# Kernel tuning notes

Measured on AMD Instinct MI355X. Metric: run time of the kernel, lower is better.

## Reference

```python
import jax, jax.numpy as jnp
import numpy as np

D_MODEL = 1024
NUM_HEADS = 16
D_HEAD = D_MODEL // NUM_HEADS
BATCH = 2
SEQ = 2048


def setup_inputs() -> dict:
    key = jax.random.key(0)
    ks = jax.random.split(key, 5)
    std = 0.02
    return {
        "x": jax.random.normal(ks[0], (BATCH, SEQ, D_MODEL), dtype=jnp.float32),
        "Wq": jax.random.normal(ks[1], (D_MODEL, D_MODEL), dtype=jnp.float32) * std,
        "Wk": jax.random.normal(ks[2], (D_MODEL, D_MODEL), dtype=jnp.float32) * std,
        "Wv": jax.random.normal(ks[3], (D_MODEL, D_MODEL), dtype=jnp.float32) * std,
        "Wo": jax.random.normal(ks[4], (D_MODEL, D_MODEL), dtype=jnp.float32) * std,
    }


def reference(x, Wq, Wk, Wv, Wo):
    batch, seq_len, d_model = x.shape
    h, dh = NUM_HEADS, D_HEAD

    def split_heads(W):
        # x @ W.T -> (b, s, d) -> (b, h, s, dh)
        p = jnp.einsum('bsd,ed->bse', x, W)
        return p.reshape(batch, seq_len, h, dh).transpose(0, 2, 1, 3)

    Q = split_heads(Wq)
    K = split_heads(Wk)
    V = split_heads(Wv)

    scale = 1.0 / jnp.sqrt(jnp.asarray(dh, dtype=x.dtype))
    scores = jnp.einsum('bhqd,bhkd->bhqk', Q, K) * scale
    causal = jnp.tril(jnp.ones((seq_len, seq_len), dtype=bool))
    scores = jnp.where(causal, scores, -jnp.inf)
    attn = jax.nn.softmax(scores, axis=-1)
    out = jnp.einsum('bhqk,bhkd->bhqd', attn, V)  # (b, h, s, dh)
    out = out.transpose(0, 2, 1, 3).reshape(batch, seq_len, d_model)
    return jnp.einsum('bsd,ed->bse', out, Wo)
```

## Files before the change

kernel.cpp:

```cpp
#include <hip/hip_runtime.h>

#define D_MODEL 1024
#define NUM_HEADS 16
#define D_HEAD 64
#define BATCH 2
#define SEQ 2048
#define MTOT (BATCH * SEQ)
#define PLANE ((size_t)MTOT * D_MODEL)
#define QSCALE 0.1803368801f

typedef unsigned short us;
typedef __bf16 bf16x8 __attribute__((ext_vector_type(8)));
typedef float floatx4 __attribute__((ext_vector_type(4)));

__device__ __forceinline__ unsigned int f2bf(float f) {
  union { float f; unsigned int i; } v; v.f = f;
  unsigned int r = v.i + 0x7FFFu + ((v.i >> 16) & 1u);
  return r >> 16;
}
__device__ __forceinline__ unsigned int f2bf_tr(float f) {
  union { float f; unsigned int i; } v; v.f = f;
  return v.i >> 16;
}

__global__ __launch_bounds__(256) void convert_all(const float* __restrict__ x,
                                                   const float* __restrict__ Wq,
                                                   const float* __restrict__ Wk,
                                                   const float* __restrict__ Wv,
                                                   const float* __restrict__ Wo,
                                                   us* __restrict__ xbf,
                                                   us* __restrict__ Wqkv,
                                                   us* __restrict__ Wobf) {
  const int i = blockIdx.x * 256 + threadIdx.x;
  const float* src;
  us* dst;
  if (i < (1 << 20)) {
    src = x + (size_t)i * 4;
    dst = xbf + (size_t)i * 4;
  } else {
    const int j = i - (1 << 20);
    const int w = j >> 18;
    const int o = j & ((1 << 18) - 1);
    if (w < 3) {
      const float* ws = (w == 0) ? Wq : (w == 1) ? Wk : Wv;
      src = ws + (size_t)o * 4;
      dst = Wqkv + (size_t)w * (D_MODEL * D_MODEL) + (size_t)o * 4;
    } else {
      src = Wo + (size_t)o * 4;
      dst = Wobf + (size_t)o * 4;
    }
  }
  float4 v = *(const float4*)src;
  uint2 pk;
  pk.x = f2bf(v.x) | (f2bf(v.y) << 16);
  pk.y = f2bf(v.z) | (f2bf(v.w) << 16);
  *(uint2*)dst = pk;
}

template <int CMODE>
__global__ __launch_bounds__(256) void gemm_mfma(const us* __restrict__ A,
                                                 const us* __restrict__ B,
                                                 void* __restrict__ Cv,
                                                 int M, int N, int K) {
  __shared__ __bf16 As[2][128 * 32];
  __shared__ __bf16 Bs[2][128 * 32];
  const int tid = threadIdx.x;
  const int wid = tid >> 6;
  const int lane = tid & 63;
  const int bm = blockIdx.y * 128;
  const int bn = blockIdx.x * 128;
  const int wm = (wid & 1) * 64;
  const int wn = (wid >> 1) * 64;
  const int lr = lane & 15;
  const int quad = lane >> 4;

  floatx4 acc[4][4] = {};
  const int cb0 = wid * 128;

  auto stage = [&](int buf, int k0) {
#pragma unroll
    for (int p = 0; p < 2; ++p) {
      const int cb = cb0 + p * 64;
      const int c = cb + lane;
      const us* ga = A + (size_t)(bm + (c >> 2)) * K + (k0 + (c & 3) * 8);
      const us* gb = B + (size_t)(bn + (c >> 2)) * K + (k0 + (c & 3) * 8);
      __builtin_amdgcn_global_load_lds((const __attribute__((address_space(1))) void*)ga,
                                       (__attribute__((address_space(3))) void*)(&As[buf][cb * 8]),
                                       16, 0, 0);
      __builtin_amdgcn_global_load_lds((const __attribute__((address_space(1))) void*)gb,
                                       (__attribute__((address_space(3))) void*)(&Bs[buf][cb * 8]),
                                       16, 0, 0);
    }
  };

  stage(0, 0);
  __syncthreads();

  int cur = 0;
  for (int k0 = 0; k0 < K; k0 += 32) {
    if (k0 + 32 < K) stage(cur ^ 1, k0 + 32);

    bf16x8 a[4], b[4];
#pragma unroll
    for (int i = 0; i < 4; ++i)
      a[i] = *(const bf16x8*)&As[cur][(wm + i * 16 + lr) * 32 + quad * 8];
#pragma unroll
    for (int j = 0; j < 4; ++j)
      b[j] = *(const bf16x8*)&Bs[cur][(wn + j * 16 + lr) * 32 + quad * 8];
#pragma unroll
    for (int i = 0; i < 4; ++i)
#pragma unroll
      for (int j = 0; j < 4; ++j)
        acc[i][j] = __builtin_amdgcn_mfma_f32_16x16x32_bf16(a[i], b[j], acc[i][j], 0, 0, 0);

    __syncthreads();
    cur ^= 1;
  }

#pragma unroll
  for (int i = 0; i < 4; ++i) {
#pragma unroll
    for (int j = 0; j < 4; ++j) {
      const int col = bn + wn + j * 16 + lr;
      if constexpr (CMODE == 1) {
        us* dst = (us*)Cv;
        const int plane = col >> 10;
        if (plane < 2) {
          const float s = (plane == 0) ? QSCALE : 1.0f;
#pragma unroll
          for (int r = 0; r < 4; ++r) {
            const int row = bm + wm + i * 16 + quad * 4 + r;
            dst[(size_t)plane * PLANE + (size_t)row * 1024 + (col & 1023)] =
                (us)f2bf(acc[i][j][r] * s);
          }
        } else {
          const int d = col & 63;
          const int hh = (col >> 6) & 15;
          const int row0 = bm + wm + i * 16 + quad * 4;
          const int bb = row0 >> 11;
          const int ss = row0 & 2047;
          uint2 pk;
          pk.x = f2bf(acc[i][j][0]) | (f2bf(acc[i][j][1]) << 16);
          pk.y = f2bf(acc[i][j][2]) | (f2bf(acc[i][j][3]) << 16);
          *(uint2*)&dst[2 * PLANE + ((size_t)((bb * 16 + hh) * 64 + d)) * 2048 + ss] = pk;
        }
      } else {
#pragma unroll
        for (int r = 0; r < 4; ++r) {
          const int row = bm + wm + i * 16 + quad * 4 + r;
          ((float*)Cv)[(size_t)row * N + col] = acc[i][j][r];
        }
      }
    }
  }
}

#define ASTR 72

__global__ __launch_bounds__(512, 2) void attn_mfma(const us* __restrict__ Qb,
                                                    const us* __restrict__ Kb,
                                                    const us* __restrict__ Vtg,
                                                    us* __restrict__ Ob) {
  const int bx = blockIdx.x;
  const int b = bx >> 8;
  const int idx = bx & 255;
  const int h = idx >> 4;
  const int s0 = idx & 15;
  const int strip = b ? (15 - s0) : s0;
  const int q0 = strip * 128;
  const int ntiles = 2 * strip + 2;
  const int tid = threadIdx.x;
  const int w = tid >> 6;
  const int lane = tid & 63;
  const int lr = lane & 15;
  const int quad = lane >> 4;

  __shared__ us Ks[2][64 * ASTR];
  __shared__ us Vs[2][64 * ASTR];
  __shared__ us Ps[8 * 16 * ASTR];

  const us* kbase = Kb + (size_t)(b * SEQ) * D_MODEL + h * D_HEAD;
  const us* vbase = Vtg + (size_t)((b * 16 + h) * 64) * 2048;
  us* const pg = &Ps[w * 16 * ASTR];

  const int grow = q0 + w * 16;
  const us* qp = Qb + (size_t)(b * SEQ + grow + lr) * D_MODEL + h * D_HEAD;
  const bf16x8 qa0 = *(const bf16x8*)(qp + quad * 8);
  const bf16x8 qa1 = *(const bf16x8*)(qp + 32 + quad * 8);

  floatx4 oacc[4] = {};
  floatx4 lacc = {};
  bf16x8 ones;
#pragma unroll
  for (int i = 0; i < 8; ++i) ones[i] = (__bf16)1.0f;

  const int srow = tid >> 3;
  const int schunk = tid & 7;

  uint4 kreg, vreg;
  kreg = *(const uint4*)(kbase + (size_t)srow * D_MODEL + schunk * 8);
  vreg = *(const uint4*)(vbase + (size_t)srow * 2048 + schunk * 8);
  *(uint4*)&Ks[0][srow * ASTR + schunk * 8] = kreg;
  *(uint4*)&Vs[0][srow * ASTR + schunk * 8] = vreg;
  __syncthreads();

  for (int t = 0; t < ntiles; ++t) {
    const int k0 = t * 64;
    const int cur = t & 1;
    const bool more = (t + 1 < ntiles);

    if (more) {
      const int kn = k0 + 64;
      kreg = *(const uint4*)(kbase + (size_t)(kn + srow) * D_MODEL + schunk * 8);
      vreg = *(const uint4*)(vbase + (size_t)srow * 2048 + kn + schunk * 8);
    }

#pragma unroll
    for (int jt = 0; jt < 4; ++jt) {
      const bf16x8 kb0 = *(const bf16x8*)&Ks[cur][(jt * 16 + lr) * ASTR + quad * 8];
      const bf16x8 kb1 = *(const bf16x8*)&Ks[cur][(jt * 16 + lr) * ASTR + 32 + quad * 8];
      floatx4 s = {};
      s = __builtin_amdgcn_mfma_f32_16x16x32_bf16(kb0, qa0, s, 0, 0, 0);
      s = __builtin_amdgcn_mfma_f32_16x16x32_bf16(kb1, qa1, s, 0, 0, 0);
      const int kb = k0 + jt * 16 + quad * 4;
      const bool needMask = (k0 + jt * 16 + 15 > grow);
      float p[4];
#pragma unroll
      for (int r = 0; r < 4; ++r) {
        float e = __builtin_amdgcn_exp2f(s[r]);
        if (needMask && (kb + r > grow + lr)) e = 0.f;
        p[r] = e;
      }
      uint2 pk;
      pk.x = f2bf_tr(p[0]) | (f2bf_tr(p[1]) << 16);
      pk.y = f2bf_tr(p[2]) | (f2bf_tr(p[3]) << 16);
      *(uint2*)&pg[lr * ASTR + jt * 16 + quad * 4] = pk;
    }

    const bf16x8 pa0 = *(const bf16x8*)&pg[lr * ASTR + quad * 8];
    const bf16x8 pa1 = *(const bf16x8*)&pg[lr * ASTR + 32 + quad * 8];
    lacc = __builtin_amdgcn_mfma_f32_16x16x32_bf16(ones, pa0, lacc, 0, 0, 0);
    lacc = __builtin_amdgcn_mfma_f32_16x16x32_bf16(ones, pa1, lacc, 0, 0, 0);
#pragma unroll
    for (int nt = 0; nt < 4; ++nt) {
      const bf16x8 vb0 = *(const bf16x8*)&Vs[cur][(nt * 16 + lr) * ASTR + quad * 8];
      const bf16x8 vb1 = *(const bf16x8*)&Vs[cur][(nt * 16 + lr) * ASTR + 32 + quad * 8];
      oacc[nt] = __builtin_amdgcn_mfma_f32_16x16x32_bf16(vb0, pa0, oacc[nt], 0, 0, 0);
      oacc[nt] = __builtin_amdgcn_mfma_f32_16x16x32_bf16(vb1, pa1, oacc[nt], 0, 0, 0);
    }

    if (more) {
      const int nxt = cur ^ 1;
      *(uint4*)&Ks[nxt][srow * ASTR + schunk * 8] = kreg;
      *(uint4*)&Vs[nxt][srow * ASTR + schunk * 8] = vreg;
    }
    __syncthreads();
  }

  const float inv = 1.f / lacc[0];
#pragma unroll
  for (int nt = 0; nt < 4; ++nt) {
    uint2 pk;
    pk.x = f2bf_tr(oacc[nt][0] * inv) | (f2bf_tr(oacc[nt][1] * inv) << 16);
    pk.y = f2bf_tr(oacc[nt][2] * inv) | (f2bf_tr(oacc[nt][3] * inv) << 16);
    *(uint2*)&pg[lr * ASTR + nt * 16 + quad * 4] = pk;
  }
#pragma unroll
  for (int p = 0; p < 2; ++p) {
    const int c = lane + 64 * p;
    *(uint4*)(Ob + (size_t)(b * SEQ + grow + (c >> 3)) * D_MODEL + h * D_HEAD + (c & 7) * 8) =
        *(const uint4*)&pg[(c >> 3) * ASTR + (c & 7) * 8];
  }
}

extern "C" void kernel_launch(void* const* d_in, const int* in_sizes, int n_in,
                              void* d_out, int out_size, void* d_ws, size_t ws_size,
                              hipStream_t stream) {
  const float* x  = (const float*)d_in[0];
  const float* Wq = (const float*)d_in[1];
  const float* Wk = (const float*)d_in[2];
  const float* Wv = (const float*)d_in[3];
  const float* Wo = (const float*)d_in[4];

  us* xbf = (us*)d_ws;
  us* Qb  = xbf + PLANE;
  us* Kb  = xbf + 2 * PLANE;
  us* Vt  = xbf + 3 * PLANE;
  us* Wobf = xbf + 4 * PLANE;
  us* Ab  = xbf;
  us* Wqkv = (us*)d_out;
  float* out = (float*)d_out;

  convert_all<<<8192, 256, 0, stream>>>(x, Wq, Wk, Wv, Wo, xbf, Wqkv, Wobf);

  gemm_mfma<1><<<dim3(3072 / 128, MTOT / 128), 256, 0, stream>>>(xbf, Wqkv, Qb, MTOT, 3072, D_MODEL);

  attn_mfma<<<512, 512, 0, stream>>>(Qb, Kb, Vt, Ab);

  gemm_mfma<2><<<dim3(D_MODEL / 128, MTOT / 128), 256, 0, stream>>>(Ab, Wobf, out, MTOT, D_MODEL, D_MODEL);
}
```

Measured before the change: 175.7 us.

## Split attention KV range across block pairs with atomic-flag combine

Each attention block now handles a 256-row query strip (two 16-row groups per wave) over half of its causal KV tiles. Two blocks share a strip, write fp32 partial outputs and row sums to workspace, and the second to finish (found through an atomic counter) adds the partner's partials and normalizes. This is meant to balance work across blocks and reuse each K/V tile load for twice as many query rows. The cost is extra global traffic for the partials, flag resets in the convert kernel, and more registers per thread under a raised occupancy hint.

```diff
diff --git a/kernel.cpp b/kernel.cpp
--- a/kernel.cpp
+++ b/kernel.cpp
@@ -30,8 +30,10 @@
                                                    const float* __restrict__ Wo,
                                                    us* __restrict__ xbf,
                                                    us* __restrict__ Wqkv,
-                                                   us* __restrict__ Wobf) {
+                                                   us* __restrict__ Wobf,
+                                                   int* __restrict__ flags) {
   const int i = blockIdx.x * 256 + threadIdx.x;
+  if (blockIdx.x == 0) flags[threadIdx.x] = 0;
   const float* src;
   us* dst;
   if (i < (1 << 20)) {
@@ -157,18 +159,25 @@
 
 #define ASTR 72
 
-__global__ __launch_bounds__(512, 2) void attn_mfma(const us* __restrict__ Qb,
+__global__ __launch_bounds__(512, 4) void attn_mfma(const us* __restrict__ Qb,
                                                     const us* __restrict__ Kb,
                                                     const us* __restrict__ Vtg,
-                                                    us* __restrict__ Ob) {
+                                                    us* __restrict__ Ob,
+                                                    float* __restrict__ Opart,
+                                                    float* __restrict__ Lpart,
+                                                    int* __restrict__ Flags) {
   const int bx = blockIdx.x;
   const int b = bx >> 8;
   const int idx = bx & 255;
   const int h = idx >> 4;
-  const int s0 = idx & 15;
-  const int strip = b ? (15 - s0) : s0;
-  const int q0 = strip * 128;
-  const int ntiles = 2 * strip + 2;
+  const int jj = idx & 15;
+  const int s0 = jj >> 1;
+  const int half = jj & 1;
+  const int strip = b ? (7 - s0) : s0;
+  const int q0 = strip * 256;
+  const int T = 4 * (strip + 1);
+  const int t0 = half * (T >> 1);
+  const int t1 = t0 + (T >> 1);
   const int tid = threadIdx.x;
   const int w = tid >> 6;
   const int lane = tid & 63;
@@ -177,19 +186,30 @@
 
   __shared__ us Ks[2][64 * ASTR];
   __shared__ us Vs[2][64 * ASTR];
-  __shared__ us Ps[8 * 16 * ASTR];
+  __shared__ us Ps[8 * 2 * 16 * ASTR];
+  __shared__ int amCombiner;
 
   const us* kbase = Kb + (size_t)(b * SEQ) * D_MODEL + h * D_HEAD;
   const us* vbase = Vtg + (size_t)((b * 16 + h) * 64) * 2048;
-  us* const pg = &Ps[w * 16 * ASTR];
-
-  const int grow = q0 + w * 16;
-  const us* qp = Qb + (size_t)(b * SEQ + grow + lr) * D_MODEL + h * D_HEAD;
-  const bf16x8 qa0 = *(const bf16x8*)(qp + quad * 8);
-  const bf16x8 qa1 = *(const bf16x8*)(qp + 32 + quad * 8);
-
-  floatx4 oacc[4] = {};
-  floatx4 lacc = {};
+  us* const pg0 = &Ps[(w * 2 + 0) * 16 * ASTR];
+  us* const pg1 = &Ps[(w * 2 + 1) * 16 * ASTR];
+
+  const size_t pairIdx = (size_t)((b * 16 + h) * 8 + strip);
+  float* const Op = Opart + (pairIdx * 2 + half) * (64 * 256);
+  float* const Lp = Lpart + (pairIdx * 2 + half) * 256;
+  const float* const pOp = Opart + (pairIdx * 2 + (half ^ 1)) * (64 * 256);
+  const float* const pLp = Lpart + (pairIdx * 2 + (half ^ 1)) * 256;
+
+  bf16x8 qa[2][2];
+#pragma unroll
+  for (int g = 0; g < 2; ++g) {
+    const us* qp = Qb + (size_t)(b * SEQ + q0 + w * 32 + g * 16 + lr) * D_MODEL + h * D_HEAD;
+    qa[g][0] = *(const bf16x8*)(qp + quad * 8);
+    qa[g][1] = *(const bf16x8*)(qp + 32 + quad * 8);
+  }
+
+  floatx4 oacc[2][4] = {};
+  floatx4 lacc[2] = {};
   bf16x8 ones;
 #pragma unroll
   for (int i = 0; i < 8; ++i) ones[i] = (__bf16)1.0f;
@@ -198,16 +218,16 @@
   const int schunk = tid & 7;
 
   uint4 kreg, vreg;
-  kreg = *(const uint4*)(kbase + (size_t)srow * D_MODEL + schunk * 8);
-  vreg = *(const uint4*)(vbase + (size_t)srow * 2048 + schunk * 8);
+  kreg = *(const uint4*)(kbase + (size_t)(t0 * 64 + srow) * D_MODEL + schunk * 8);
+  vreg = *(const uint4*)(vbase + (size_t)srow * 2048 + t0 * 64 + schunk * 8);
   *(uint4*)&Ks[0][srow * ASTR + schunk * 8] = kreg;
   *(uint4*)&Vs[0][srow * ASTR + schunk * 8] = vreg;
   __syncthreads();
 
-  for (int t = 0; t < ntiles; ++t) {
+  for (int t = t0; t < t1; ++t) {
     const int k0 = t * 64;
-    const int cur = t & 1;
-    const bool more = (t + 1 < ntiles);
+    const int cur = (t - t0) & 1;
+    const bool more = (t + 1 < t1);
 
     if (more) {
       const int kn = k0 + 64;
@@ -219,34 +239,45 @@
     for (int jt = 0; jt < 4; ++jt) {
       const bf16x8 kb0 = *(const bf16x8*)&Ks[cur][(jt * 16 + lr) * ASTR + quad * 8];
       const bf16x8 kb1 = *(const bf16x8*)&Ks[cur][(jt * 16 + lr) * ASTR + 32 + quad * 8];
-      floatx4 s = {};
-      s = __builtin_amdgcn_mfma_f32_16x16x32_bf16(kb0, qa0, s, 0, 0, 0);
-      s = __builtin_amdgcn_mfma_f32_16x16x32_bf16(kb1, qa1, s, 0, 0, 0);
-      const int kb = k0 + jt * 16 + quad * 4;
-      const bool needMask = (k0 + jt * 16 + 15 > grow);
-      float p[4];
-#pragma unroll
-      for (int r = 0; r < 4; ++r) {
-        float e = __builtin_amdgcn_exp2f(s[r]);
-        if (needMask && (kb + r > grow + lr)) e = 0.f;
-        p[r] = e;
+#pragma unroll
+      for (int g = 0; g < 2; ++g) {
+        floatx4 s = {};
+        s = __builtin_amdgcn_mfma_f32_16x16x32_bf16(kb0, qa[g][0], s, 0, 0, 0);
+        s = __builtin_amdgcn_mfma_f32_16x16x32_bf16(kb1, qa[g][1], s, 0, 0, 0);
+        const int grow = q0 + w * 32 + g * 16;
+        const int kb = k0 + jt * 16 + quad * 4;
+        const bool needMask = (k0 + jt * 16 + 15 > grow);
+        float p[4];
+#pragma unroll
+        for (int r = 0; r < 4; ++r) {
+          float e = __builtin_amdgcn_exp2f(s[r]);
+          if (needMask && (kb + r > grow + lr)) e = 0.f;
+          p[r] = e;
+        }
+        uint2 pk;
+        pk.x = f2bf_tr(p[0]) | (f2bf_tr(p[1]) << 16);
+        pk.y = f2bf_tr(p[2]) | (f2bf_tr(p[3]) << 16);
+        us* const pg = g ? pg1 : pg0;
+        *(uint2*)&pg[lr * ASTR + jt * 16 + quad * 4] = pk;
       }
-      uint2 pk;
-      pk.x = f2bf_tr(p[0]) | (f2bf_tr(p[1]) << 16);
-      pk.y = f2bf_tr(p[2]) | (f2bf_tr(p[3]) << 16);
-      *(uint2*)&pg[lr * ASTR + jt * 16 + quad * 4] = pk;
-    }
-
-    const bf16x8 pa0 = *(const bf16x8*)&pg[lr * ASTR + quad * 8];
-    const bf16x8 pa1 = *(const bf16x8*)&pg[lr * ASTR + 32 + quad * 8];
-    lacc = __builtin_amdgcn_mfma_f32_16x16x32_bf16(ones, pa0, lacc, 0, 0, 0);
-    lacc = __builtin_amdgcn_mfma_f32_16x16x32_bf16(ones, pa1, lacc, 0, 0, 0);
+    }
+
+    const bf16x8 pa00 = *(const bf16x8*)&pg0[lr * ASTR + quad * 8];
+    const bf16x8 pa01 = *(const bf16x8*)&pg0[lr * ASTR + 32 + quad * 8];
+    const bf16x8 pa10 = *(const bf16x8*)&pg1[lr * ASTR + quad * 8];
+    const bf16x8 pa11 = *(const bf16x8*)&pg1[lr * ASTR + 32 + quad * 8];
+    lacc[0] = __builtin_amdgcn_mfma_f32_16x16x32_bf16(ones, pa00, lacc[0], 0, 0, 0);
+    lacc[0] = __builtin_amdgcn_mfma_f32_16x16x32_bf16(ones, pa01, lacc[0], 0, 0, 0);
+    lacc[1] = __builtin_amdgcn_mfma_f32_16x16x32_bf16(ones, pa10, lacc[1], 0, 0, 0);
+    lacc[1] = __builtin_amdgcn_mfma_f32_16x16x32_bf16(ones, pa11, lacc[1], 0, 0, 0);
 #pragma unroll
     for (int nt = 0; nt < 4; ++nt) {
       const bf16x8 vb0 = *(const bf16x8*)&Vs[cur][(nt * 16 + lr) * ASTR + quad * 8];
       const bf16x8 vb1 = *(const bf16x8*)&Vs[cur][(nt * 16 + lr) * ASTR + 32 + quad * 8];
-      oacc[nt] = __builtin_amdgcn_mfma_f32_16x16x32_bf16(vb0, pa0, oacc[nt], 0, 0, 0);
-      oacc[nt] = __builtin_amdgcn_mfma_f32_16x16x32_bf16(vb1, pa1, oacc[nt], 0, 0, 0);
+      oacc[0][nt] = __builtin_amdgcn_mfma_f32_16x16x32_bf16(vb0, pa00, oacc[0][nt], 0, 0, 0);
+      oacc[0][nt] = __builtin_amdgcn_mfma_f32_16x16x32_bf16(vb1, pa01, oacc[0][nt], 0, 0, 0);
+      oacc[1][nt] = __builtin_amdgcn_mfma_f32_16x16x32_bf16(vb0, pa10, oacc[1][nt], 0, 0, 0);
+      oacc[1][nt] = __builtin_amdgcn_mfma_f32_16x16x32_bf16(vb1, pa11, oacc[1][nt], 0, 0, 0);
     }
 
     if (more) {
@@ -257,19 +288,52 @@
     __syncthreads();
   }
 
-  const float inv = 1.f / lacc[0];
-#pragma unroll
-  for (int nt = 0; nt < 4; ++nt) {
-    uint2 pk;
-    pk.x = f2bf_tr(oacc[nt][0] * inv) | (f2bf_tr(oacc[nt][1] * inv) << 16);
-    pk.y = f2bf_tr(oacc[nt][2] * inv) | (f2bf_tr(oacc[nt][3] * inv) << 16);
-    *(uint2*)&pg[lr * ASTR + nt * 16 + quad * 4] = pk;
-  }
-#pragma unroll
-  for (int p = 0; p < 2; ++p) {
-    const int c = lane + 64 * p;
-    *(uint4*)(Ob + (size_t)(b * SEQ + grow + (c >> 3)) * D_MODEL + h * D_HEAD + (c & 7) * 8) =
-        *(const uint4*)&pg[(c >> 3) * ASTR + (c & 7) * 8];
+#pragma unroll
+  for (int g = 0; g < 2; ++g) {
+    const int rowb = w * 32 + g * 16;
+#pragma unroll
+    for (int nt = 0; nt < 4; ++nt)
+#pragma unroll
+      for (int r = 0; r < 4; ++r)
+        Op[(size_t)(nt * 16 + quad * 4 + r) * 256 + rowb + lr] = oacc[g][nt][r];
+    if (quad == 0) Lp[rowb + lr] = lacc[g][0];
+  }
+  __syncthreads();
+
+  if (tid == 0) {
+    const int old = __hip_atomic_fetch_add(&Flags[pairIdx], 1, __ATOMIC_ACQ_REL,
+                                           __HIP_MEMORY_SCOPE_AGENT);
+    amCombiner = (old == 1);
+  }
+  __syncthreads();
+  if (!amCombiner) return;
+
+#pragma unroll
+  for (int g = 0; g < 2; ++g) {
+    const int rowb = w * 32 + g * 16;
+    const float lsum = lacc[g][0] + pLp[rowb + lr];
+    const float inv = 1.f / lsum;
+#pragma unroll
+    for (int nt = 0; nt < 4; ++nt)
+#pragma unroll
+      for (int r = 0; r < 4; ++r)
+        oacc[g][nt][r] += pOp[(size_t)(nt * 16 + quad * 4 + r) * 256 + rowb + lr];
+
+    us* const pg = g ? pg1 : pg0;
+    const int grow = q0 + rowb;
+#pragma unroll
+    for (int nt = 0; nt < 4; ++nt) {
+      uint2 pk;
+      pk.x = f2bf_tr(oacc[g][nt][0] * inv) | (f2bf_tr(oacc[g][nt][1] * inv) << 16);
+      pk.y = f2bf_tr(oacc[g][nt][2] * inv) | (f2bf_tr(oacc[g][nt][3] * inv) << 16);
+      *(uint2*)&pg[lr * ASTR + nt * 16 + quad * 4] = pk;
+    }
+#pragma unroll
+    for (int p = 0; p < 2; ++p) {
+      const int c = lane + 64 * p;
+      *(uint4*)(Ob + (size_t)(b * SEQ + grow + (c >> 3)) * D_MODEL + h * D_HEAD + (c & 7) * 8) =
+          *(const uint4*)&pg[(c >> 3) * ASTR + (c & 7) * 8];
+    }
   }
 }
 
@@ -287,15 +351,18 @@
   us* Kb  = xbf + 2 * PLANE;
   us* Vt  = xbf + 3 * PLANE;
   us* Wobf = xbf + 4 * PLANE;
+  float* Opart = (float*)(xbf + 4 * PLANE + (1 << 20));
+  float* Lpart = Opart + (size_t)256 * 2 * 64 * 256;
+  int* Flags   = (int*)(Lpart + 256 * 2 * 256);
   us* Ab  = xbf;
   us* Wqkv = (us*)d_out;
   float* out = (float*)d_out;
 
-  convert_all<<<8192, 256, 0, stream>>>(x, Wq, Wk, Wv, Wo, xbf, Wqkv, Wobf);
+  convert_all<<<8192, 256, 0, stream>>>(x, Wq, Wk, Wv, Wo, xbf, Wqkv, Wobf, Flags);
 
   gemm_mfma<1><<<dim3(3072 / 128, MTOT / 128), 256, 0, stream>>>(xbf, Wqkv, Qb, MTOT, 3072, D_MODEL);
 
-  attn_mfma<<<512, 512, 0, stream>>>(Qb, Kb, Vt, Ab);
+  attn_mfma<<<512, 512, 0, stream>>>(Qb, Kb, Vt, Ab, Opart, Lpart, Flags);
 
   gemm_mfma<2><<<dim3(D_MODEL / 128, MTOT / 128), 256, 0, stream>>>(Ab, Wobf, out, MTOT, D_MODEL, D_MODEL);
 }
```

Measured after the change: 195.8 us. 1.11x slower.
